# Kernel tuning notes

Hardware: AMD Instinct MI355X
Metric: run time of the kernel (lower is better)

The kernel has to match this reference:

```python
import jax, jax.numpy as jnp
import numpy as np

K = 16  # neighborhood size


def _eigen_ratio(pts, k):
    """pts: [B, N, 3] -> ratio lambda_max / lambda_mid per point, [B, N]."""
    pts = pts[..., :3]
    # pairwise squared distances [B, N, N]
    sq = jnp.sum(pts * pts, axis=-1)  # [B, N]
    d2 = sq[:, :, None] + sq[:, None, :] - 2.0 * jnp.einsum('bnd,bmd->bnm', pts, pts)
    # k nearest neighbors (self included, as in KNN(x, x))
    _, idx = jax.lax.top_k(-d2, k)  # idx: [B, N, k] int32
    # gather neighbor coordinates: [B, N, k, 3]
    neighbors = jax.vmap(lambda p, i: p[i])(pts, idx)
    mean = jnp.mean(neighbors, axis=2, keepdims=True)
    diff = neighbors - mean  # [B, N, k, 3]
    # covariance = mean over k of outer products -> [B, N, 3, 3]
    cov = jnp.einsum('bnki,bnkj->bnij', diff, diff) / k
    ev = jnp.linalg.eigvalsh(cov)  # ascending: [..., 3]
    return ev[..., 2] / ev[..., 1]


def setup_inputs() -> dict:
    key = jax.random.key(0)
    kx, ky = jax.random.split(key)
    x = jax.random.normal(kx, (2, 8192, 3), dtype=jnp.float32)
    y = jax.random.normal(ky, (2, 8192, 3), dtype=jnp.float32)
    return {"x": x, "y": y}


def reference(x, y):
    er1 = _eigen_ratio(x, K)  # [B, N]
    er2 = _eigen_ratio(y, K)
    res = jnp.mean((er1 - er2) ** 2, axis=-1)  # mean over points
    return jnp.mean(res)  # reduction='mean' over batch
```

## Files before the change

### kernel.cpp

```cpp
#include <hip/hip_runtime.h>
#include <hip/hip_bf16.h>
#include <math.h>

#define NPTS   8192
#define KNN    16
#define G      16
#define NCELL  (G * G * G)
#define NCHUNK 128
#define NPART  4

__constant__ float c_B[17] = {
    -1e30f,
    -1.5341205f, -1.1503494f, -0.8871466f, -0.6744898f, -0.4887764f,
    -0.3186394f, -0.1573107f,  0.0f,        0.1573107f,  0.3186394f,
     0.4887764f,  0.6744898f,  0.8871466f,  1.1503494f,  1.5341205f,
     1e30f
};

__device__ __forceinline__ int cellOf(float v) {
    int c = 0;
#pragma unroll
    for (int i = 1; i <= 15; ++i) c += (v >= c_B[i]) ? 1 : 0;
    return c;
}

__device__ __forceinline__ int spread3(int v) {
    v = (v | (v << 4)) & 0x0C3;
    v = (v | (v << 2)) & 0x249;
    return v;
}

__device__ __forceinline__ int mortonCell(float px, float py, float pz) {
    return (spread3(cellOf(px)) << 2) | (spread3(cellOf(py)) << 1) | spread3(cellOf(pz));
}

__device__ __forceinline__ float dpp_prev_f(float v) {
    int r = __builtin_amdgcn_update_dpp(0, __float_as_int(v), 0x111, 0xF, 0xF, false);
    return __int_as_float(r);
}
__device__ __forceinline__ int dpp_prev_i(int v) {
    return __builtin_amdgcn_update_dpp(0, v, 0x111, 0xF, 0xF, false);
}

__device__ __forceinline__ float sum16(float v) {
    int b;
    b = __builtin_amdgcn_update_dpp(0, __float_as_int(v), 0xB1, 0xF, 0xF, false);
    v += __int_as_float(b);
    b = __builtin_amdgcn_update_dpp(0, __float_as_int(v), 0x4E, 0xF, 0xF, false);
    v += __int_as_float(b);
    b = __builtin_amdgcn_update_dpp(0, __float_as_int(v), 0x141, 0xF, 0xF, false);
    v += __int_as_float(b);
    b = __builtin_amdgcn_update_dpp(0, __float_as_int(v), 0x140, 0xF, 0xF, false);
    v += __int_as_float(b);
    return v;
}

__global__ __launch_bounds__(1024) void countscan_kernel(
    const float* __restrict__ x, const float* __restrict__ y,
    unsigned int* __restrict__ cellcnt ) {

    __shared__ unsigned int h[NCELL];
    __shared__ unsigned int scanbuf[1024];
    const int tid   = threadIdx.x;
    const int cloud = blockIdx.x;
    const float* __restrict__ src = (cloud < 2 ? x : y) + (size_t)(cloud & 1) * NPTS * 3;

    for (int i = tid; i < NCELL; i += 1024) h[i] = 0;
    __syncthreads();
#pragma unroll
    for (int k = 0; k < 8; ++k) {
        int p = (k << 10) | tid;
        atomicAdd(&h[mortonCell(src[3 * p], src[3 * p + 1], src[3 * p + 2])], 1u);
    }
    __syncthreads();

    unsigned int c0 = h[4 * tid], c1 = h[4 * tid + 1];
    unsigned int c2 = h[4 * tid + 2], c3 = h[4 * tid + 3];
    unsigned int ssum = c0 + c1 + c2 + c3;
    scanbuf[tid] = ssum;
    __syncthreads();
    for (int d = 1; d < 1024; d <<= 1) {
        unsigned int a = scanbuf[tid];
        unsigned int w = (tid >= d) ? scanbuf[tid - d] : 0;
        __syncthreads();
        scanbuf[tid] = a + w;
        __syncthreads();
    }
    unsigned int excl = scanbuf[tid] - ssum;
    unsigned int* cc = cellcnt + cloud * NCELL;
    cc[4 * tid]     = excl;
    cc[4 * tid + 1] = excl + c0;
    cc[4 * tid + 2] = excl + c0 + c1;
    cc[4 * tid + 3] = excl + c0 + c1 + c2;
}

__global__ __launch_bounds__(256) void scatter_kernel(
    const float* __restrict__ x, const float* __restrict__ y,
    unsigned int* __restrict__ cellcnt,
    float4* __restrict__ Ps, unsigned short* __restrict__ origids) {

    const int tid   = threadIdx.x;
    const int cloud = blockIdx.x >> 2;
    const int part  = blockIdx.x & 3;
    const float* __restrict__ src = (cloud < 2 ? x : y) + (size_t)(cloud & 1) * NPTS * 3;
    unsigned int* cc = cellcnt + cloud * NCELL;

#pragma unroll
    for (int k = 0; k < 8; ++k) {
        int p = (part << 11) | (k << 8) | tid;
        float px = src[3 * p], py = src[3 * p + 1], pz = src[3 * p + 2];
        int c = mortonCell(px, py, pz);
        unsigned int pos = atomicAdd(&cc[c], 1u);
        Ps[(cloud << 13) + pos] = make_float4(-2.f * px, -2.f * py, -2.f * pz,
                                              px * px + py * py + pz * pz);
        origids[(cloud << 13) + pos] = (unsigned short)p;
    }
}

__global__ __launch_bounds__(256) void aabb_kernel(
    const float4* __restrict__ Ps, float* __restrict__ aabbG ) {

    const int tid  = threadIdx.x;
    const int lane = tid & 63;
    const int w    = (blockIdx.x << 2) | (tid >> 6);
    const int cloud = w >> 7;
    const int c     = w & 127;

    float4 f = Ps[(cloud << 13) | (c << 6) | lane];
    float px = -0.5f * f.x, py = -0.5f * f.y, pz = -0.5f * f.z;
    float lx = px, hx = px, ly = py, hy = py, lz = pz, hz = pz;
#pragma unroll
    for (int s = 1; s < 64; s <<= 1) {
        lx = fminf(lx, __shfl_xor(lx, s)); hx = fmaxf(hx, __shfl_xor(hx, s));
        ly = fminf(ly, __shfl_xor(ly, s)); hy = fmaxf(hy, __shfl_xor(hy, s));
        lz = fminf(lz, __shfl_xor(lz, s)); hz = fmaxf(hz, __shfl_xor(hz, s));
    }
    if (lane == 0) {
        float* ab = aabbG + cloud * (6 * NCHUNK);
        ab[0 * NCHUNK + c] = lx; ab[1 * NCHUNK + c] = hx;
        ab[2 * NCHUNK + c] = ly; ab[3 * NCHUNK + c] = hy;
        ab[4 * NCHUNK + c] = lz; ab[5 * NCHUNK + c] = hz;
    }
}

__global__ __launch_bounds__(64) void knn_cov_kernel(
    const float4* __restrict__ Ps, const unsigned short* __restrict__ origids,
    const float* __restrict__ aabbG, float* __restrict__ cov) {

    const int lane = threadIdx.x;
    const int wid  = blockIdx.x;
    const int cloud = wid >> 13;
    const int s     = wid & (NPTS - 1);

    const float4* __restrict__ Pc = Ps + (cloud << 13);
    const float* __restrict__ ab = aabbG + cloud * (6 * NCHUNK);
    const float4 qp = Pc[s];
    const float sqq = qp.w;
    const float qx = -0.5f * qp.x, qy = -0.5f * qp.y, qz = -0.5f * qp.z;
    const int co = s >> 6;

    float bval[2];
#pragma unroll
    for (int g = 0; g < 2; ++g) {
        int c = (g << 6) | lane;
        float dxl = fmaxf(0.f, fmaxf(ab[c] - qx, qx - ab[NCHUNK + c]));
        float dyl = fmaxf(0.f, fmaxf(ab[2 * NCHUNK + c] - qy, qy - ab[3 * NCHUNK + c]));
        float dzl = fmaxf(0.f, fmaxf(ab[4 * NCHUNK + c] - qz, qz - ab[5 * NCHUNK + c]));
        bval[g] = dxl * dxl + dyl * dyl + dzl * dzl;
    }
    unsigned long long rem0 = ~0ull, rem1 = ~0ull;
    if (co < 64) rem0 &= ~(1ull << co); else rem1 &= ~(1ull << (co - 64));

    auto dual_argmin = [&](unsigned long long live0, unsigned long long live1,
                           int& cidA, int& cidB, bool& hasB) {
        unsigned int k0 = ((live0 >> lane) & 1)
            ? ((__float_as_uint(bval[0]) & 0xFFFFFF80u) | (unsigned)lane) : 0xFFFFFFFFu;
        unsigned int k1 = ((live1 >> lane) & 1)
            ? ((__float_as_uint(bval[1]) & 0xFFFFFF80u) | (unsigned)(64 + lane)) : 0xFFFFFFFFu;
        unsigned int a = min(k0, k1), b = max(k0, k1);
#pragma unroll
        for (int w = 1; w < 64; w <<= 1) {
            unsigned int oa = __shfl_xor(a, w);
            unsigned int ob = __shfl_xor(b, w);
            unsigned int mn = min(a, oa), mx = max(a, oa);
            unsigned int c2 = (a < oa) ? b : ob;
            a = mn; b = min(mx, c2);
        }
        cidA = (int)(a & 127u);
        hasB = (b != 0xFFFFFFFFu); cidB = (int)(b & 127u);
    };
    auto clear_rem = [&](int cid) {
        if (cid < 64) rem0 &= ~(1ull << cid); else rem1 &= ~(1ull << (cid - 64));
    };
    auto bound_of = [&](int cid) {
        return __int_as_float(__builtin_amdgcn_readlane(
            __float_as_int(bval[cid >> 6]), cid & 63));
    };

    int pA, pB; bool hB;
    dual_argmin(rem0, rem1, pA, pB, hB);
    clear_rem(pA); clear_rem(pB);
    float4 pfA = Pc[(pA << 6) | lane];
    float4 pfB = Pc[(pB << 6) | lane];

    float valV, thr;
    int   idxV;
    {
        int pos = (co << 6) | lane;
        float4 f = Pc[pos];
        float k = fmaf(qx, f.x, fmaf(qy, f.y, fmaf(qz, f.z, sqq + f.w)));
        int p = pos;
#pragma unroll
        for (int size = 2; size <= 64; size <<= 1) {
#pragma unroll
            for (int stride = size >> 1; stride >= 1; stride >>= 1) {
                float ok = __shfl_xor(k, stride);
                int   op = __shfl_xor(p, stride);
                bool up = ((lane & size) == 0);
                bool lower = ((lane & stride) == 0);
                bool want_min = (up == lower);
                bool take = want_min ? (ok < k) : (ok > k);
                k = take ? ok : k;
                p = take ? op : p;
            }
        }
        valV = __shfl(k, lane & 15);
        idxV = __shfl(p, lane & 15);
        thr  = __shfl(k, 15);
    }

    auto process = [&](float4 f, int cid) {
        float d2 = fmaf(qx, f.x, fmaf(qy, f.y, fmaf(qz, f.z, sqq + f.w)));
        unsigned long long m = __ballot(d2 < thr);
        if (m) {
            do {
                int li = __builtin_ctzll(m); m &= m - 1;
                float sv = __int_as_float(
                    __builtin_amdgcn_readlane(__float_as_int(d2), li));
                int sj = (cid << 6) | li;
                float pv = dpp_prev_f(valV);
                int   pi = dpp_prev_i(idxV);
                bool keep  = (valV <= sv);
                bool fromv = ((lane & 15) == 0) || (pv <= sv);
                float nv = keep ? valV : (fromv ? sv : pv);
                int   ni = keep ? idxV : (fromv ? sj : pi);
                valV = nv; idxV = ni;
            } while (m);
            thr = __int_as_float(__builtin_amdgcn_readlane(__float_as_int(valV), 15));
        }
    };

    if (bound_of(pA) < thr) process(pfA, pA);
    if (bound_of(pB) < thr) process(pfB, pB);

    for (;;) {
        unsigned long long live0 = rem0 & __ballot(bval[0] < thr);
        unsigned long long live1 = rem1 & __ballot(bval[1] < thr);
        if (!(live0 | live1)) break;

        int cidA, cidB; bool hasB;
        if (__popcll(live0) + __popcll(live1) <= 2) {
            if (live0) { cidA = __builtin_ctzll(live0); live0 &= live0 - 1; }
            else       { cidA = 64 + __builtin_ctzll(live1); live1 &= live1 - 1; }
            if (live0)      { cidB = __builtin_ctzll(live0); hasB = true; }
            else if (live1) { cidB = 64 + __builtin_ctzll(live1); hasB = true; }
            else hasB = false;
        } else {
            dual_argmin(live0, live1, cidA, cidB, hasB);
        }
        clear_rem(cidA);
        if (hasB) clear_rem(cidB);

        float4 fA = Pc[(cidA << 6) | lane];
        float4 fB;
        if (hasB) fB = Pc[(cidB << 6) | lane];

        process(fA, cidA);
        if (hasB && bound_of(cidB) < thr) process(fB, cidB);
    }

    float4 nf = Pc[idxV];
    float nx = -0.5f * nf.x, ny = -0.5f * nf.y, nz = -0.5f * nf.z;

    const float invk = 1.0f / KNN;
    float mx = sum16(nx) * invk;
    float my = sum16(ny) * invk;
    float mz = sum16(nz) * invk;

    float dx = nx - mx, dy = ny - my, dz = nz - mz;
    float c00 = sum16(dx * dx) * invk, c01 = sum16(dx * dy) * invk, c02 = sum16(dx * dz) * invk;
    float c11 = sum16(dy * dy) * invk, c12 = sum16(dy * dz) * invk, c22 = sum16(dz * dz) * invk;

    if (lane == 0) {
        int orig = origids[(cloud << 13) + s];
        float* cp = cov + ((size_t)(cloud << 13) + orig) * 6;
        *(float2*)(cp)     = make_float2(c00, c01);
        *(float2*)(cp + 2) = make_float2(c02, c11);
        *(float2*)(cp + 4) = make_float2(c12, c22);
    }
}

__device__ double eig_ratio(const float* __restrict__ cp) {
    double a00 = cp[0], a01 = cp[1], a02 = cp[2];
    double a11 = cp[3], a12 = cp[4], a22 = cp[5];

    double qm = (a00 + a11 + a22) * (1.0 / 3.0);
    double p1 = a01 * a01 + a02 * a02 + a12 * a12;
    double b00 = a00 - qm, b11 = a11 - qm, b22 = a22 - qm;
    double p2 = b00 * b00 + b11 * b11 + b22 * b22 + 2.0 * p1;

    if (p2 <= 0.0) return 1.0;
    double p = sqrt(p2 * (1.0 / 6.0));
    double inv = 1.0 / p;
    double m00 = b00 * inv, m11 = b11 * inv, m22 = b22 * inv;
    double m01 = a01 * inv, m02 = a02 * inv, m12 = a12 * inv;
    double detB = m00 * (m11 * m22 - m12 * m12)
                - m01 * (m01 * m22 - m12 * m02)
                + m02 * (m01 * m12 - m11 * m02);
    double r = 0.5 * detB;
    r = fmin(1.0, fmax(-1.0, r));
    double phi = acos(r) * (1.0 / 3.0);
    double e1 = qm + 2.0 * p * cos(phi);
    double e3 = qm + 2.0 * p * cos(phi + 2.0943951023931953);
    double e2 = 3.0 * qm - e1 - e3;
    return e1 / e2;
}

__global__ __launch_bounds__(256) void eigred_kernel(const float* __restrict__ cov,
                                                     double* __restrict__ partial) {
    __shared__ double sb[256];
    const int i = blockIdx.x * 256 + threadIdx.x;
    double r1 = eig_ratio(cov + (size_t)i * 6);
    double r2 = eig_ratio(cov + (size_t)(2 * NPTS + i) * 6);
    double d = r1 - r2;
    sb[threadIdx.x] = d * d;
    __syncthreads();
    for (int s2 = 128; s2 > 0; s2 >>= 1) {
        if (threadIdx.x < s2) sb[threadIdx.x] += sb[threadIdx.x + s2];
        __syncthreads();
    }
    if (threadIdx.x == 0) partial[blockIdx.x] = sb[0];
}

__global__ __launch_bounds__(64) void final_kernel(const double* __restrict__ partial,
                                                   float* __restrict__ out) {
    double v = partial[threadIdx.x];
#pragma unroll
    for (int w = 1; w < 64; w <<= 1) v += __shfl_xor(v, w);
    if (threadIdx.x == 0) out[0] = (float)(v / (double)(2 * NPTS));
}

extern "C" void kernel_launch(void* const* d_in, const int* in_sizes, int n_in,
                              void* d_out, int out_size, void* d_ws, size_t ws_size,
                              hipStream_t stream) {
    const float* x = (const float*)d_in[0];
    const float* y = (const float*)d_in[1];
    char* ws = (char*)d_ws;

    float4*         Ps      = (float4*)(ws);
    unsigned short* origids = (unsigned short*)(ws + 524288);
    float*          aabbG   = (float*)(ws + 589824);
    float*          cov     = (float*)(ws + 602112);
    unsigned int*   cellcnt = (unsigned int*)(ws + 1388544);
    double*         partial = (double*)(ws + 1454080);
    float*          out     = (float*)d_out;

    countscan_kernel<<<4, 1024, 0, stream>>>(x, y, cellcnt);
    scatter_kernel<<<4 * NPART, 256, 0, stream>>>(x, y, cellcnt, Ps, origids);
    aabb_kernel<<<128, 256, 0, stream>>>(Ps, aabbG);
    knn_cov_kernel<<<4 * NPTS, 64, 0, stream>>>(Ps, origids, aabbG, cov);
    eigred_kernel<<<64, 256, 0, stream>>>(cov, partial);
    final_kernel<<<1, 64, 0, stream>>>(partial, out);
}
```

Baseline: 90.08 us.

## Fuse count, scan, scatter and AABB into one build kernel; two waves per knn block

Merges the cell counting/scan, scatter and AABB kernels into a single 4-block build kernel. Points are kept in registers and the prefix offsets stay in shared memory, which removes two launches and the global cellcnt round trip. The knn kernel now packs two query waves per 128-thread block, halving the block count. The cost is that the scatter and AABB work now runs on only 4 blocks instead of 16 and 128, so less of it runs in parallel.

```diff
diff --git a/kernel.cpp b/kernel.cpp
--- a/kernel.cpp
+++ b/kernel.cpp
@@ -7,7 +7,6 @@
 #define G      16
 #define NCELL  (G * G * G)
 #define NCHUNK 128
-#define NPART  4
 
 __constant__ float c_B[17] = {
     -1e30f,
@@ -55,22 +54,29 @@
     return v;
 }
 
-__global__ __launch_bounds__(1024) void countscan_kernel(
+__global__ __launch_bounds__(1024) void build_kernel(
     const float* __restrict__ x, const float* __restrict__ y,
-    unsigned int* __restrict__ cellcnt ) {
+    float4* __restrict__ Ps, unsigned short* __restrict__ origids,
+    float* __restrict__ aabbG ) {
 
     __shared__ unsigned int h[NCELL];
     __shared__ unsigned int scanbuf[1024];
+
     const int tid   = threadIdx.x;
     const int cloud = blockIdx.x;
     const float* __restrict__ src = (cloud < 2 ? x : y) + (size_t)(cloud & 1) * NPTS * 3;
 
     for (int i = tid; i < NCELL; i += 1024) h[i] = 0;
     __syncthreads();
+
+    float px[8], py[8], pz[8];
+    int   cel[8];
 #pragma unroll
     for (int k = 0; k < 8; ++k) {
         int p = (k << 10) | tid;
-        atomicAdd(&h[mortonCell(src[3 * p], src[3 * p + 1], src[3 * p + 2])], 1u);
+        px[k] = src[3 * p]; py[k] = src[3 * p + 1]; pz[k] = src[3 * p + 2];
+        cel[k] = mortonCell(px[k], py[k], pz[k]);
+        atomicAdd(&h[cel[k]], 1u);
     }
     __syncthreads();
 
@@ -87,68 +93,48 @@
         __syncthreads();
     }
     unsigned int excl = scanbuf[tid] - ssum;
-    unsigned int* cc = cellcnt + cloud * NCELL;
-    cc[4 * tid]     = excl;
-    cc[4 * tid + 1] = excl + c0;
-    cc[4 * tid + 2] = excl + c0 + c1;
-    cc[4 * tid + 3] = excl + c0 + c1 + c2;
-}
-
-__global__ __launch_bounds__(256) void scatter_kernel(
-    const float* __restrict__ x, const float* __restrict__ y,
-    unsigned int* __restrict__ cellcnt,
-    float4* __restrict__ Ps, unsigned short* __restrict__ origids) {
-
-    const int tid   = threadIdx.x;
-    const int cloud = blockIdx.x >> 2;
-    const int part  = blockIdx.x & 3;
-    const float* __restrict__ src = (cloud < 2 ? x : y) + (size_t)(cloud & 1) * NPTS * 3;
-    unsigned int* cc = cellcnt + cloud * NCELL;
+    h[4 * tid]     = excl;
+    h[4 * tid + 1] = excl + c0;
+    h[4 * tid + 2] = excl + c0 + c1;
+    h[4 * tid + 3] = excl + c0 + c1 + c2;
+    __syncthreads();
 
 #pragma unroll
     for (int k = 0; k < 8; ++k) {
-        int p = (part << 11) | (k << 8) | tid;
-        float px = src[3 * p], py = src[3 * p + 1], pz = src[3 * p + 2];
-        int c = mortonCell(px, py, pz);
-        unsigned int pos = atomicAdd(&cc[c], 1u);
-        Ps[(cloud << 13) + pos] = make_float4(-2.f * px, -2.f * py, -2.f * pz,
-                                              px * px + py * py + pz * pz);
+        int p = (k << 10) | tid;
+        unsigned int pos = atomicAdd(&h[cel[k]], 1u);
+        Ps[(cloud << 13) + pos] = make_float4(-2.f * px[k], -2.f * py[k], -2.f * pz[k],
+                                              px[k] * px[k] + py[k] * py[k] + pz[k] * pz[k]);
         origids[(cloud << 13) + pos] = (unsigned short)p;
     }
-}
-
-__global__ __launch_bounds__(256) void aabb_kernel(
-    const float4* __restrict__ Ps, float* __restrict__ aabbG ) {
-
-    const int tid  = threadIdx.x;
-    const int lane = tid & 63;
-    const int w    = (blockIdx.x << 2) | (tid >> 6);
-    const int cloud = w >> 7;
-    const int c     = w & 127;
-
-    float4 f = Ps[(cloud << 13) | (c << 6) | lane];
-    float px = -0.5f * f.x, py = -0.5f * f.y, pz = -0.5f * f.z;
-    float lx = px, hx = px, ly = py, hy = py, lz = pz, hz = pz;
-#pragma unroll
-    for (int s = 1; s < 64; s <<= 1) {
-        lx = fminf(lx, __shfl_xor(lx, s)); hx = fmaxf(hx, __shfl_xor(hx, s));
-        ly = fminf(ly, __shfl_xor(ly, s)); hy = fmaxf(hy, __shfl_xor(hy, s));
-        lz = fminf(lz, __shfl_xor(lz, s)); hz = fmaxf(hz, __shfl_xor(hz, s));
-    }
-    if (lane == 0) {
-        float* ab = aabbG + cloud * (6 * NCHUNK);
-        ab[0 * NCHUNK + c] = lx; ab[1 * NCHUNK + c] = hx;
-        ab[2 * NCHUNK + c] = ly; ab[3 * NCHUNK + c] = hy;
-        ab[4 * NCHUNK + c] = lz; ab[5 * NCHUNK + c] = hz;
-    }
-}
-
-__global__ __launch_bounds__(64) void knn_cov_kernel(
+    __syncthreads();
+
+    const int wv = tid >> 6, lane = tid & 63;
+    for (int c = wv; c < NCHUNK; c += 16) {
+        float4 f = Ps[(cloud << 13) | (c << 6) | lane];
+        float ax = -0.5f * f.x, ay = -0.5f * f.y, az = -0.5f * f.z;
+        float lx = ax, hx = ax, ly = ay, hy = ay, lz = az, hz = az;
+#pragma unroll
+        for (int s = 1; s < 64; s <<= 1) {
+            lx = fminf(lx, __shfl_xor(lx, s)); hx = fmaxf(hx, __shfl_xor(hx, s));
+            ly = fminf(ly, __shfl_xor(ly, s)); hy = fmaxf(hy, __shfl_xor(hy, s));
+            lz = fminf(lz, __shfl_xor(lz, s)); hz = fmaxf(hz, __shfl_xor(hz, s));
+        }
+        if (lane == 0) {
+            float* ab = aabbG + cloud * (6 * NCHUNK);
+            ab[0 * NCHUNK + c] = lx; ab[1 * NCHUNK + c] = hx;
+            ab[2 * NCHUNK + c] = ly; ab[3 * NCHUNK + c] = hy;
+            ab[4 * NCHUNK + c] = lz; ab[5 * NCHUNK + c] = hz;
+        }
+    }
+}
+
+__global__ __launch_bounds__(128) void knn_cov_kernel(
     const float4* __restrict__ Ps, const unsigned short* __restrict__ origids,
     const float* __restrict__ aabbG, float* __restrict__ cov) {
 
-    const int lane = threadIdx.x;
-    const int wid  = blockIdx.x;
+    const int lane = threadIdx.x & 63;
+    const int wid  = (blockIdx.x << 1) | (threadIdx.x >> 6);
     const int cloud = wid >> 13;
     const int s     = wid & (NPTS - 1);
 
@@ -361,14 +347,11 @@
     unsigned short* origids = (unsigned short*)(ws + 524288);
     float*          aabbG   = (float*)(ws + 589824);
     float*          cov     = (float*)(ws + 602112);
-    unsigned int*   cellcnt = (unsigned int*)(ws + 1388544);
-    double*         partial = (double*)(ws + 1454080);
+    double*         partial = (double*)(ws + 1388544);
     float*          out     = (float*)d_out;
 
-    countscan_kernel<<<4, 1024, 0, stream>>>(x, y, cellcnt);
-    scatter_kernel<<<4 * NPART, 256, 0, stream>>>(x, y, cellcnt, Ps, origids);
-    aabb_kernel<<<128, 256, 0, stream>>>(Ps, aabbG);
-    knn_cov_kernel<<<4 * NPTS, 64, 0, stream>>>(Ps, origids, aabbG, cov);
+    build_kernel<<<4, 1024, 0, stream>>>(x, y, Ps, origids, aabbG);
+    knn_cov_kernel<<<2 * NPTS, 128, 0, stream>>>(Ps, origids, aabbG, cov);
     eigred_kernel<<<64, 256, 0, stream>>>(cov, partial);
     final_kernel<<<1, 64, 0, stream>>>(partial, out);
 }
```

After: 102.9 us. +14.2%, slower.

## Process up to four candidate chunks per KNN iteration and fuse final reduction

Applied to the files above, without the earlier changes.

The KNN search loop now pops two pairs of live chunks per iteration, loading up to four chunks' points before processing them, so more global loads are in flight at once and fewer ballot/argmin rounds are needed. A last-block pattern with an atomic counter folds the final reduction into the eigen kernel, removing one launch. The counter is reset by the first block of the knn kernel. Extra prefetching raises register use and may process chunks that a tighter threshold would have pruned.

```diff
diff --git a/kernel.cpp b/kernel.cpp
--- a/kernel.cpp
+++ b/kernel.cpp
@@ -145,12 +145,15 @@
 
 __global__ __launch_bounds__(64) void knn_cov_kernel(
     const float4* __restrict__ Ps, const unsigned short* __restrict__ origids,
-    const float* __restrict__ aabbG, float* __restrict__ cov) {
+    const float* __restrict__ aabbG, float* __restrict__ cov,
+    unsigned int* __restrict__ counter) {
 
     const int lane = threadIdx.x;
     const int wid  = blockIdx.x;
     const int cloud = wid >> 13;
     const int s     = wid & (NPTS - 1);
+
+    if (wid == 0 && lane == 0) *counter = 0;
 
     const float4* __restrict__ Pc = Ps + (cloud << 13);
     const float* __restrict__ ab = aabbG + cloud * (6 * NCHUNK);
@@ -171,11 +174,11 @@
     unsigned long long rem0 = ~0ull, rem1 = ~0ull;
     if (co < 64) rem0 &= ~(1ull << co); else rem1 &= ~(1ull << (co - 64));
 
-    auto dual_argmin = [&](unsigned long long live0, unsigned long long live1,
+    auto dual_argmin = [&](unsigned long long l0, unsigned long long l1,
                            int& cidA, int& cidB, bool& hasB) {
-        unsigned int k0 = ((live0 >> lane) & 1)
+        unsigned int k0 = ((l0 >> lane) & 1)
             ? ((__float_as_uint(bval[0]) & 0xFFFFFF80u) | (unsigned)lane) : 0xFFFFFFFFu;
-        unsigned int k1 = ((live1 >> lane) & 1)
+        unsigned int k1 = ((l1 >> lane) & 1)
             ? ((__float_as_uint(bval[1]) & 0xFFFFFF80u) | (unsigned)(64 + lane)) : 0xFFFFFFFFu;
         unsigned int a = min(k0, k1), b = max(k0, k1);
 #pragma unroll
@@ -196,10 +199,26 @@
         return __int_as_float(__builtin_amdgcn_readlane(
             __float_as_int(bval[cid >> 6]), cid & 63));
     };
-
-    int pA, pB; bool hB;
-    dual_argmin(rem0, rem1, pA, pB, hB);
-    clear_rem(pA); clear_rem(pB);
+    auto popPair = [&](unsigned long long& l0, unsigned long long& l1,
+                       int& cA, int& cB, bool& hB) {
+        if (__popcll(l0) + __popcll(l1) <= 2) {
+            if (l0) { cA = __builtin_ctzll(l0); l0 &= l0 - 1; }
+            else    { cA = 64 + __builtin_ctzll(l1); l1 &= l1 - 1; }
+            if (l0)      { cB = __builtin_ctzll(l0); l0 &= l0 - 1; hB = true; }
+            else if (l1) { cB = 64 + __builtin_ctzll(l1); l1 &= l1 - 1; hB = true; }
+            else hB = false;
+        } else {
+            dual_argmin(l0, l1, cA, cB, hB);
+            if (cA < 64) l0 &= ~(1ull << cA); else l1 &= ~(1ull << (cA - 64));
+            if (hB) { if (cB < 64) l0 &= ~(1ull << cB); else l1 &= ~(1ull << (cB - 64)); }
+        }
+        clear_rem(cA);
+        if (hB) clear_rem(cB);
+    };
+
+    unsigned long long t0 = rem0, t1 = rem1;
+    int pA, pB; bool hPB;
+    popPair(t0, t1, pA, pB, hPB);
     float4 pfA = Pc[(pA << 6) | lane];
     float4 pfB = Pc[(pB << 6) | lane];
 
@@ -251,32 +270,28 @@
     };
 
     if (bound_of(pA) < thr) process(pfA, pA);
-    if (bound_of(pB) < thr) process(pfB, pB);
+    if (hPB && bound_of(pB) < thr) process(pfB, pB);
 
     for (;;) {
         unsigned long long live0 = rem0 & __ballot(bval[0] < thr);
         unsigned long long live1 = rem1 & __ballot(bval[1] < thr);
         if (!(live0 | live1)) break;
 
-        int cidA, cidB; bool hasB;
-        if (__popcll(live0) + __popcll(live1) <= 2) {
-            if (live0) { cidA = __builtin_ctzll(live0); live0 &= live0 - 1; }
-            else       { cidA = 64 + __builtin_ctzll(live1); live1 &= live1 - 1; }
-            if (live0)      { cidB = __builtin_ctzll(live0); hasB = true; }
-            else if (live1) { cidB = 64 + __builtin_ctzll(live1); hasB = true; }
-            else hasB = false;
-        } else {
-            dual_argmin(live0, live1, cidA, cidB, hasB);
-        }
-        clear_rem(cidA);
-        if (hasB) clear_rem(cidB);
+        int cidA, cidB, cidC = 0, cidD = 0;
+        bool hasB, hasC = false, hasD = false;
+        popPair(live0, live1, cidA, cidB, hasB);
+        if (live0 | live1) { popPair(live0, live1, cidC, cidD, hasD); hasC = true; }
 
         float4 fA = Pc[(cidA << 6) | lane];
-        float4 fB;
+        float4 fB, fC, fD;
         if (hasB) fB = Pc[(cidB << 6) | lane];
+        if (hasC) fC = Pc[(cidC << 6) | lane];
+        if (hasD) fD = Pc[(cidD << 6) | lane];
 
         process(fA, cidA);
         if (hasB && bound_of(cidB) < thr) process(fB, cidB);
+        if (hasC && bound_of(cidC) < thr) process(fC, cidC);
+        if (hasD && bound_of(cidD) < thr) process(fD, cidD);
     }
 
     float4 nf = Pc[idxV];
@@ -326,9 +341,14 @@
     return e1 / e2;
 }
 
+#define EIG_BLOCKS 64
+
 __global__ __launch_bounds__(256) void eigred_kernel(const float* __restrict__ cov,
-                                                     double* __restrict__ partial) {
+                                                     double* __restrict__ partial,
+                                                     unsigned int* __restrict__ counter,
+                                                     float* __restrict__ out) {
     __shared__ double sb[256];
+    __shared__ bool islast;
     const int i = blockIdx.x * 256 + threadIdx.x;
     double r1 = eig_ratio(cov + (size_t)i * 6);
     double r2 = eig_ratio(cov + (size_t)(2 * NPTS + i) * 6);
@@ -339,15 +359,19 @@
         if (threadIdx.x < s2) sb[threadIdx.x] += sb[threadIdx.x + s2];
         __syncthreads();
     }
-    if (threadIdx.x == 0) partial[blockIdx.x] = sb[0];
-}
-
-__global__ __launch_bounds__(64) void final_kernel(const double* __restrict__ partial,
-                                                   float* __restrict__ out) {
-    double v = partial[threadIdx.x];
-#pragma unroll
-    for (int w = 1; w < 64; w <<= 1) v += __shfl_xor(v, w);
-    if (threadIdx.x == 0) out[0] = (float)(v / (double)(2 * NPTS));
+    if (threadIdx.x == 0) {
+        partial[blockIdx.x] = sb[0];
+        __threadfence();
+        islast = (atomicAdd(counter, 1u) == EIG_BLOCKS - 1);
+    }
+    __syncthreads();
+    if (islast && threadIdx.x < 64) {
+        __threadfence();
+        double v = ((volatile double*)partial)[threadIdx.x];
+#pragma unroll
+        for (int w = 1; w < 64; w <<= 1) v += __shfl_xor(v, w);
+        if (threadIdx.x == 0) out[0] = (float)(v / (double)(2 * NPTS));
+    }
 }
 
 extern "C" void kernel_launch(void* const* d_in, const int* in_sizes, int n_in,
@@ -363,12 +387,12 @@
     float*          cov     = (float*)(ws + 602112);
     unsigned int*   cellcnt = (unsigned int*)(ws + 1388544);
     double*         partial = (double*)(ws + 1454080);
+    unsigned int*   counter = (unsigned int*)(ws + 1454592);
     float*          out     = (float*)d_out;
 
     countscan_kernel<<<4, 1024, 0, stream>>>(x, y, cellcnt);
     scatter_kernel<<<4 * NPART, 256, 0, stream>>>(x, y, cellcnt, Ps, origids);
     aabb_kernel<<<128, 256, 0, stream>>>(Ps, aabbG);
-    knn_cov_kernel<<<4 * NPTS, 64, 0, stream>>>(Ps, origids, aabbG, cov);
-    eigred_kernel<<<64, 256, 0, stream>>>(cov, partial);
-    final_kernel<<<1, 64, 0, stream>>>(partial, out);
-}
+    knn_cov_kernel<<<4 * NPTS, 64, 0, stream>>>(Ps, origids, aabbG, cov, counter);
+    eigred_kernel<<<EIG_BLOCKS, 256, 0, stream>>>(cov, partial, counter, out);
+}
```

New measurement: 92.87 us. +3.1%, slower.
